# Performance work log

Measured on AMD Instinct MI355X. Metric: run time of the kernel, lower is better.

## Reference

```python
import jax, jax.numpy as jnp
import numpy as np

B, S, D, H = 2, 2048, 1024, 16
DK = D // H


def setup_inputs() -> dict:
    key = jax.random.key(0)
    ks = jax.random.split(key, 12)
    q = jax.random.normal(ks[0], (B, S, D), dtype=jnp.float32)
    k = jax.random.normal(ks[1], (B, S, D), dtype=jnp.float32)
    v = jax.random.normal(ks[2], (B, S, D), dtype=jnp.float32)
    # causal mask: 1 = attend, 0 = masked (masked_fill(mask==0, -inf))
    mask = jnp.tril(jnp.ones((S, S), dtype=jnp.int32))[None, None]
    w = 0.02
    Wq = jax.random.normal(ks[3], (D, D), dtype=jnp.float32) * w
    bq = jnp.zeros((D,), dtype=jnp.float32)
    Wk = jax.random.normal(ks[4], (D, D), dtype=jnp.float32) * w
    bk = jnp.zeros((D,), dtype=jnp.float32)
    Wv = jax.random.normal(ks[5], (D, D), dtype=jnp.float32) * w
    bv = jnp.zeros((D,), dtype=jnp.float32)
    Wo = jax.random.normal(ks[6], (D, D), dtype=jnp.float32) * w
    bo = jnp.zeros((D,), dtype=jnp.float32)
    return {"q": q, "k": k, "v": v, "mask": mask,
            "Wq": Wq, "bq": bq, "Wk": Wk, "bk": bk,
            "Wv": Wv, "bv": bv, "Wo": Wo, "bo": bo}


def _split_heads(x):
    b, s, _ = x.shape
    return x.reshape(b, s, H, DK).transpose(0, 2, 1, 3)  # [B,H,S,DK]


def reference(q, k, v, mask, Wq, bq, Wk, bk, Wv, bv, Wo, bo):
    qh = _split_heads(q @ Wq.T + bq)
    kh = _split_heads(k @ Wk.T + bk)
    vh = _split_heads(v @ Wv.T + bv)
    scale = 1.0 / jnp.sqrt(jnp.float32(DK))
    scores = jnp.einsum("bhqd,bhkd->bhqk", qh, kh) * scale  # [B,H,S,S]
    scores = jnp.where(mask == 0, -jnp.inf, scores)
    pesos = jax.nn.softmax(scores, axis=-1)
    pesos = jnp.nan_to_num(pesos, nan=0.0)  # fully-masked rows -> 0
    out = jnp.einsum("bhqk,bhkd->bhqd", pesos, vh)
    out = out.transpose(0, 2, 1, 3).reshape(q.shape[0], q.shape[1], D)
    # dropout is identity at inference
    return out @ Wo.T + bo
```

## Files before the change

kernel.cpp:

```cpp
#include <hip/hip_runtime.h>
#include <hip/hip_bf16.h>

#define B_  2
#define S_  2048
#define D_  1024
#define H_  16
#define DK_ 64

using bf16 = __hip_bfloat16;
typedef __bf16 bf16x8 __attribute__((ext_vector_type(8)));
typedef float  f32x4  __attribute__((ext_vector_type(4)));
typedef float  f32x16 __attribute__((ext_vector_type(16)));

__device__ inline void st1(float* p, float v) { *p = v; }
__device__ inline void st1(bf16*  p, float v) { *p = __float2bfloat16(v); }

__device__ inline void gll16(const bf16* g, bf16* l) {
    __builtin_amdgcn_global_load_lds(
        (const __attribute__((address_space(1))) unsigned int*)g,
        (__attribute__((address_space(3))) unsigned int*)l, 16, 0, 0);
}

__device__ inline f32x16 mfma32(bf16x8 a, bf16x8 b, f32x16 c) {
    return __builtin_amdgcn_mfma_f32_32x32x16_bf16(a, b, c, 0, 0, 0);
}

__device__ inline unsigned cvtpk(float lo, float hi) {
    unsigned r;
    asm("v_cvt_pk_bf16_f32 %0, %1, %2" : "=v"(r) : "v"(lo), "v"(hi));
    return r;
}

__device__ inline void plswap(unsigned &d, unsigned &s) {
    asm volatile("v_permlane32_swap_b32 %0, %1" : "+v"(d), "+v"(s));
}

__global__ __launch_bounds__(256) void cvt_kernel(
    const float* __restrict__ s0, const float* __restrict__ s1,
    const float* __restrict__ s2, const float* __restrict__ s3,
    const float* __restrict__ s4, const float* __restrict__ s5,
    const float* __restrict__ s6,
    bf16* __restrict__ d0, bf16* __restrict__ d1, bf16* __restrict__ d2,
    bf16* __restrict__ d3, bf16* __restrict__ d4, bf16* __restrict__ d5,
    bf16* __restrict__ d6, int nbig, int nsmall)
{
    const int z = blockIdx.y;
    const float* s; bf16* d; int n;
    switch (z) {
        case 0: s = s0; d = d0; n = nbig;   break;
        case 1: s = s1; d = d1; n = nbig;   break;
        case 2: s = s2; d = d2; n = nbig;   break;
        case 3: s = s3; d = d3; n = nsmall; break;
        case 4: s = s4; d = d4; n = nsmall; break;
        case 5: s = s5; d = d5; n = nsmall; break;
        default: s = s6; d = d6; n = nsmall; break;
    }
    const int idx = (blockIdx.x * 256 + threadIdx.x) * 4;
    if (idx < n) {
        const float4 v = *reinterpret_cast<const float4*>(s + idx);
        union { ushort4 u; __bf16 h[4]; } r;
        r.h[0] = (__bf16)v.x; r.h[1] = (__bf16)v.y;
        r.h[2] = (__bf16)v.z; r.h[3] = (__bf16)v.w;
        *reinterpret_cast<ushort4*>(d + idx) = r.u;
    }
}

template <typename TC, bool VT3, int BM>
__global__ __launch_bounds__(256, BM == 128 ? 3 : 4) void gemm_bt_kernel(
    const bf16* __restrict__ A0, const bf16* __restrict__ A1, const bf16* __restrict__ A2,
    const bf16* __restrict__ W0, const bf16* __restrict__ W1, const bf16* __restrict__ W2,
    const float* __restrict__ b0, const float* __restrict__ b1, const float* __restrict__ b2,
    TC* __restrict__ C0, TC* __restrict__ C1, TC* __restrict__ C2,
    int M, int N, int K)
{
    const int bid  = blockIdx.x;
    const int ny   = M / BM;
    const int tile = (bid & 7) * (gridDim.x >> 3) + (bid >> 3);
    const int x    = tile & 7;
    const int pair = tile >> 3;
    const int y    = pair % ny;
    const int z    = pair / ny;

    const bf16*  A    = (z == 0) ? A0 : (z == 1) ? A1 : A2;
    const bf16*  W    = (z == 0) ? W0 : (z == 1) ? W1 : W2;
    const float* bias = (z == 0) ? b0 : (z == 1) ? b1 : b2;
    TC*          C    = (z == 0) ? C0 : (z == 1) ? C1 : C2;

    __shared__ bf16 As[2][BM][32];
    __shared__ bf16 Bs[2][128][32];

    const int t    = threadIdx.x;
    const int lane = t & 63;
    const int wave = t >> 6;
    const int quad = lane >> 4;
    const int l16  = lane & 15;
    const int wm   = wave >> 1;
    const int wn   = wave & 1;

    const int m0 = y * BM;
    const int n0 = x * 128;

    constexpr int RPW = BM / 4;
    constexpr int MI  = BM / 32;
    const int ar0 = wave * RPW + (lane >> 2);
    const int br0 = wave * 32  + (lane >> 2);
    const int c0  = (lane & 3) * 8;
    const bf16* Ab = A + (size_t)(m0 + ar0) * K + c0;
    const bf16* Bb = W + (size_t)(n0 + br0) * K + c0;

    f32x4 acc[MI][4] = {};

    for (int kt = 0; kt < K; kt += 64) {
        __syncthreads();
#pragma unroll
        for (int hh = 0; hh < 2; hh++) {
            const int ko = kt + 32 * hh;
            gll16(Ab + ko, &As[hh][wave * RPW][0]);
            if constexpr (BM == 128) gll16(Ab + 16 * K + ko, &As[hh][wave * RPW + 16][0]);
            gll16(Bb + ko, &Bs[hh][wave * 32][0]);
            gll16(Bb + 16 * K + ko, &Bs[hh][wave * 32 + 16][0]);
        }
        __syncthreads();

#pragma unroll
        for (int hh = 0; hh < 2; hh++) {
            bf16x8 af[MI], bfr[4];
#pragma unroll
            for (int mi = 0; mi < MI; mi++)
                af[mi] = *reinterpret_cast<const bf16x8*>(&As[hh][wm * (BM / 2) + mi * 16 + l16][quad * 8]);
#pragma unroll
            for (int ni = 0; ni < 4; ni++)
                bfr[ni] = *reinterpret_cast<const bf16x8*>(&Bs[hh][wn * 64 + ni * 16 + l16][quad * 8]);
#pragma unroll
            for (int mi = 0; mi < MI; mi++)
#pragma unroll
                for (int ni = 0; ni < 4; ni++)
                    acc[mi][ni] = __builtin_amdgcn_mfma_f32_16x16x32_bf16(
                        af[mi], bfr[ni], acc[mi][ni], 0, 0, 0);
        }
    }

    if (VT3 && z == 2) {
#pragma unroll
        for (int ni = 0; ni < 4; ni++) {
            const int col = n0 + wn * 64 + ni * 16 + l16;
            const float bvv = bias[col];
            const int hh = col >> 6, dh = col & 63;
#pragma unroll
            for (int mi = 0; mi < MI; mi++) {
                const int rb  = m0 + wm * (BM / 2) + mi * 16 + quad * 4;
                const int bb  = rb >> 11;
                const int tok = rb & (S_ - 1);
                union { ushort4 u; __bf16 h[4]; } pk;
#pragma unroll
                for (int i = 0; i < 4; i++)
                    pk.h[i] = (__bf16)(acc[mi][ni][i] + bvv);
                bf16* vt = (bf16*)C + ((size_t)(bb * H_ + hh) * DK_ + dh) * S_ + tok;
                *reinterpret_cast<ushort4*>(vt) = pk.u;
            }
        }
    } else {
#pragma unroll
        for (int ni = 0; ni < 4; ni++) {
            const int col = n0 + wn * 64 + ni * 16 + l16;
            const float bvv = bias[col];
#pragma unroll
            for (int mi = 0; mi < MI; mi++) {
#pragma unroll
                for (int i = 0; i < 4; i++) {
                    const int row = m0 + wm * (BM / 2) + mi * 16 + quad * 4 + i;
                    st1(&C[(size_t)row * N + col], acc[mi][ni][i] + bvv);
                }
            }
        }
    }
}

__global__ __launch_bounds__(256, 2) void attn_kernel(
    const bf16* __restrict__ Qp, const bf16* __restrict__ Kp,
    const bf16* __restrict__ VT, bf16* __restrict__ AO)
{
    const int t    = threadIdx.x;
    const int lane = t & 63;
    const int wave = t >> 6;
    const int r31  = lane & 31;
    const int hl   = lane >> 5;
    const int l7   = lane & 7;

    const int bid = blockIdx.x;
    int til, hb;
    if (bid < 256) { til = 15 - (bid >> 5); hb = bid & 31; }
    else           { til = (bid - 256) >> 5; hb = (bid - 256) & 31; }
    const int h = hb & 15;
    const int b = hb >> 4;
    const size_t bh = (size_t)b * S_ * D_ + (size_t)h * DK_;
    const bf16* vtb = VT + (size_t)(b * H_ + h) * DK_ * S_;

    __shared__ bf16 Ks[2][2][64][64];
    __shared__ bf16 Vs[2][2][64][64];

    const int sR  = lane >> 3;
    const int scg = ((lane & 7) ^ sR) * 8;

    const float QSC = 0.18033688f;
    const float NEG = -1e30f;

    bf16x8 ONES;
#pragma unroll
    for (int j = 0; j < 8; j++) ONES[j] = (__bf16)1.0f;

    const int ntot = til + 1;

    bf16x8 qf[4];
    {
        const bf16* qr = Qp + bh + (size_t)(til * 128 + wave * 32 + r31) * D_ + 8 * hl;
#pragma unroll
        for (int d = 0; d < 4; d++) {
            qf[d] = *reinterpret_cast<const bf16x8*>(qr + 16 * d);
#pragma unroll
            for (int j = 0; j < 8; j++) qf[d][j] = (__bf16)((float)qf[d][j] * QSC);
        }
    }

    f32x16 oacc0 = {}, oacc1 = {}, lacc = {};

    auto stage = [&](int slot) {
        const int k0n = slot * 128;
        const int bb  = slot & 1;
#pragma unroll
        for (int half = 0; half < 2; half++) {
            const int kh = k0n + 64 * half;
#pragma unroll
            for (int j = 0; j < 2; j++) {
                const int rb = wave * 16 + j * 8;
                gll16(Kp + bh + (size_t)(kh + rb + sR) * D_ + scg, &Ks[bb][half][rb][0]);
                gll16(vtb + (size_t)(rb + sR) * S_ + kh + scg,     &Vs[bb][half][rb][0]);
            }
        }
    };

    stage(0);
    asm volatile("s_waitcnt vmcnt(0)" ::: "memory");
    __builtin_amdgcn_s_barrier();

    for (int it = 0; it < ntot; it++) {
        if (it + 1 < ntot) stage(it + 1);

        const int buf = it & 1;
        const int qw0 = til * 128 + wave * 32;

#pragma unroll
        for (int hh = 0; hh < 2; hh++) {
            const int k0 = it * 128 + 64 * hh;
            if (k0 > qw0 + 31) continue;

            f32x16 s0 = {}, s1 = {};
#pragma unroll
            for (int d = 0; d < 4; d++) {
                const int g = ((2 * d + hl) ^ l7) * 8;
                const bf16x8 kf0 = *reinterpret_cast<const bf16x8*>(&Ks[buf][hh][r31][g]);
                const bf16x8 kf1 = *reinterpret_cast<const bf16x8*>(&Ks[buf][hh][32 + r31][g]);
                s0 = mfma32(kf0, qf[d], s0);
                s1 = mfma32(kf1, qf[d], s1);
            }

            if (k0 + 63 > qw0) {
                const int qg = qw0 + r31;
                const int kb = k0 + 4 * hl;
#pragma unroll
                for (int r = 0; r < 16; r++) {
                    const int ko = (r & 3) + 8 * (r >> 2);
                    s0[r] = (kb + ko      <= qg) ? s0[r] : NEG;
                    s1[r] = (kb + 32 + ko <= qg) ? s1[r] : NEG;
                }
            }

#pragma unroll
            for (int r = 0; r < 16; r++) {
                s0[r] = __builtin_amdgcn_exp2f(s0[r]);
                s1[r] = __builtin_amdgcn_exp2f(s1[r]);
            }

            bf16x8 pa[4];
#pragma unroll
            for (int G = 0; G < 2; G++) {
#pragma unroll
                for (int tt = 0; tt < 2; tt++) {
                    unsigned a01, a23, a45, a67;
                    if (G == 0) {
                        a01 = cvtpk(s0[8*tt+0], s0[8*tt+1]);
                        a23 = cvtpk(s0[8*tt+2], s0[8*tt+3]);
                        a45 = cvtpk(s0[8*tt+4], s0[8*tt+5]);
                        a67 = cvtpk(s0[8*tt+6], s0[8*tt+7]);
                    } else {
                        a01 = cvtpk(s1[8*tt+0], s1[8*tt+1]);
                        a23 = cvtpk(s1[8*tt+2], s1[8*tt+3]);
                        a45 = cvtpk(s1[8*tt+4], s1[8*tt+5]);
                        a67 = cvtpk(s1[8*tt+6], s1[8*tt+7]);
                    }
                    plswap(a01, a45);
                    plswap(a23, a67);
                    union { unsigned u[4]; bf16x8 v; } pu;
                    pu.u[0] = a01; pu.u[1] = a23; pu.u[2] = a45; pu.u[3] = a67;
                    pa[2 * G + tt] = pu.v;
                }
            }

#pragma unroll
            for (int s = 0; s < 4; s++) {
                const int g = ((2 * s + hl) ^ l7) * 8;
                const bf16x8 vf0 = *reinterpret_cast<const bf16x8*>(&Vs[buf][hh][r31][g]);
                const bf16x8 vf1 = *reinterpret_cast<const bf16x8*>(&Vs[buf][hh][32 + r31][g]);
                oacc0 = mfma32(pa[s], vf0, oacc0);
                oacc1 = mfma32(pa[s], vf1, oacc1);
                lacc  = mfma32(pa[s], ONES, lacc);
            }
        }

        asm volatile("s_waitcnt vmcnt(0)" ::: "memory");
        __builtin_amdgcn_s_barrier();
    }

    {
        const int qb0 = til * 128 + wave * 32;
#pragma unroll
        for (int r = 0; r < 16; r++) {
            const int q = qb0 + (r & 3) + 8 * (r >> 2) + 4 * hl;
            const float inv = 1.0f / lacc[r];
            AO[bh + (size_t)q * D_ + r31]      = __float2bfloat16(oacc0[r] * inv);
            AO[bh + (size_t)q * D_ + 32 + r31] = __float2bfloat16(oacc1[r] * inv);
        }
    }
}

extern "C" void kernel_launch(void* const* d_in, const int* in_sizes, int n_in,
                              void* d_out, int out_size, void* d_ws, size_t ws_size,
                              hipStream_t stream)
{
    const float* q  = (const float*)d_in[0];
    const float* k  = (const float*)d_in[1];
    const float* v  = (const float*)d_in[2];
    const float* Wq = (const float*)d_in[4];
    const float* bq = (const float*)d_in[5];
    const float* Wk = (const float*)d_in[6];
    const float* bk = (const float*)d_in[7];
    const float* Wv = (const float*)d_in[8];
    const float* bv = (const float*)d_in[9];
    const float* Wo = (const float*)d_in[10];
    const float* bo = (const float*)d_in[11];
    float* out = (float*)d_out;

    bf16* ws = (bf16*)d_ws;
    const size_t MD = (size_t)(B_ * S_) * D_;
    const size_t WN = (size_t)D_ * D_;
    bf16* qb  = ws;
    bf16* kb  = ws + MD;
    bf16* vb  = ws + 2 * MD;
    bf16* wqb = ws + 3 * MD;
    bf16* wkb = wqb + WN;
    bf16* wvb = wkb + WN;
    bf16* wob = wvb + WN;
    bf16* Qp  = wob + WN;
    bf16* Kp  = Qp + MD;
    bf16* VT  = Kp + MD;
    bf16* AO  = Qp;

    const int M = B_ * S_;

    cvt_kernel<<<dim3((int)(MD / 4 / 256), 7), 256, 0, stream>>>(
        q, k, v, Wq, Wk, Wv, Wo, qb, kb, vb, wqb, wkb, wvb, wob,
        (int)MD, (int)WN);

    gemm_bt_kernel<bf16, true, 128><<<dim3(768), 256, 0, stream>>>(
        qb, kb, vb, wqb, wkb, wvb, bq, bk, bv, Qp, Kp, VT, M, D_, D_);

    attn_kernel<<<dim3(512), 256, 0, stream>>>(Qp, Kp, VT, AO);

    gemm_bt_kernel<float, false, 64><<<dim3(512), 256, 0, stream>>>(
        AO, AO, AO, wob, wob, wob, bo, bo, bo, out, out, out, M, D_, D_);
}
```

Measured before the change: 216.9 us.

## Fuse fp32-to-bf16 activation conversion into QKV projection GEMM loads

The QKV projection GEMM now loads the fp32 q/k/v activations straight into LDS through global_load_lds, using an XOR-swizzled column layout. It converts them to bf16 in registers with v_cvt_pk_bf16_f32 just before the MFMA. The conversion kernel now handles only the four weight matrices, which removes a full write and re-read pass over the three large activation tensors. In exchange the A tile in LDS doubles in size, which may reduce occupancy, and each fragment read adds extra LDS reads and convert instructions.

```diff
diff --git a/kernel.cpp b/kernel.cpp
--- a/kernel.cpp
+++ b/kernel.cpp
@@ -15,7 +15,7 @@
 __device__ inline void st1(float* p, float v) { *p = v; }
 __device__ inline void st1(bf16*  p, float v) { *p = __float2bfloat16(v); }
 
-__device__ inline void gll16(const bf16* g, bf16* l) {
+__device__ inline void gll16(const void* g, void* l) {
     __builtin_amdgcn_global_load_lds(
         (const __attribute__((address_space(1))) unsigned int*)g,
         (__attribute__((address_space(3))) unsigned int*)l, 16, 0, 0);
@@ -38,22 +38,16 @@
 __global__ __launch_bounds__(256) void cvt_kernel(
     const float* __restrict__ s0, const float* __restrict__ s1,
     const float* __restrict__ s2, const float* __restrict__ s3,
-    const float* __restrict__ s4, const float* __restrict__ s5,
-    const float* __restrict__ s6,
-    bf16* __restrict__ d0, bf16* __restrict__ d1, bf16* __restrict__ d2,
-    bf16* __restrict__ d3, bf16* __restrict__ d4, bf16* __restrict__ d5,
-    bf16* __restrict__ d6, int nbig, int nsmall)
+    bf16* __restrict__ d0, bf16* __restrict__ d1,
+    bf16* __restrict__ d2, bf16* __restrict__ d3, int n)
 {
     const int z = blockIdx.y;
-    const float* s; bf16* d; int n;
+    const float* s; bf16* d;
     switch (z) {
-        case 0: s = s0; d = d0; n = nbig;   break;
-        case 1: s = s1; d = d1; n = nbig;   break;
-        case 2: s = s2; d = d2; n = nbig;   break;
-        case 3: s = s3; d = d3; n = nsmall; break;
-        case 4: s = s4; d = d4; n = nsmall; break;
-        case 5: s = s5; d = d5; n = nsmall; break;
-        default: s = s6; d = d6; n = nsmall; break;
+        case 0: s = s0; d = d0; break;
+        case 1: s = s1; d = d1; break;
+        case 2: s = s2; d = d2; break;
+        default: s = s3; d = d3; break;
     }
     const int idx = (blockIdx.x * 256 + threadIdx.x) * 4;
     if (idx < n) {
@@ -65,14 +59,16 @@
     }
 }
 
-template <typename TC, bool VT3, int BM>
+template <typename TA, typename TC, bool VT3, int BM>
 __global__ __launch_bounds__(256, BM == 128 ? 3 : 4) void gemm_bt_kernel(
-    const bf16* __restrict__ A0, const bf16* __restrict__ A1, const bf16* __restrict__ A2,
+    const TA* __restrict__ A0, const TA* __restrict__ A1, const TA* __restrict__ A2,
     const bf16* __restrict__ W0, const bf16* __restrict__ W1, const bf16* __restrict__ W2,
     const float* __restrict__ b0, const float* __restrict__ b1, const float* __restrict__ b2,
     TC* __restrict__ C0, TC* __restrict__ C1, TC* __restrict__ C2,
     int M, int N, int K)
 {
+    constexpr bool AF32 = (sizeof(TA) == 4);
+
     const int bid  = blockIdx.x;
     const int ny   = M / BM;
     const int tile = (bid & 7) * (gridDim.x >> 3) + (bid >> 3);
@@ -81,12 +77,12 @@
     const int y    = pair % ny;
     const int z    = pair / ny;
 
-    const bf16*  A    = (z == 0) ? A0 : (z == 1) ? A1 : A2;
+    const TA*    A    = (z == 0) ? A0 : (z == 1) ? A1 : A2;
     const bf16*  W    = (z == 0) ? W0 : (z == 1) ? W1 : W2;
     const float* bias = (z == 0) ? b0 : (z == 1) ? b1 : b2;
     TC*          C    = (z == 0) ? C0 : (z == 1) ? C1 : C2;
 
-    __shared__ bf16 As[2][BM][32];
+    __shared__ TA   As[2][BM][32];
     __shared__ bf16 Bs[2][128][32];
 
     const int t    = threadIdx.x;
@@ -102,11 +98,13 @@
 
     constexpr int RPW = BM / 4;
     constexpr int MI  = BM / 32;
-    const int ar0 = wave * RPW + (lane >> 2);
-    const int br0 = wave * 32  + (lane >> 2);
-    const int c0  = (lane & 3) * 8;
-    const bf16* Ab = A + (size_t)(m0 + ar0) * K + c0;
-    const bf16* Bb = W + (size_t)(n0 + br0) * K + c0;
+    int ar0, ac0;
+    if constexpr (AF32) { ar0 = wave * RPW + (lane >> 3); ac0 = ((lane & 7) ^ (lane >> 3)) * 4; }
+    else                { ar0 = wave * RPW + (lane >> 2); ac0 = (lane & 3) * 8; }
+    const int br0 = wave * 32 + (lane >> 2);
+    const int bc0 = (lane & 3) * 8;
+    const TA*   Ab = A + (size_t)(m0 + ar0) * K + ac0;
+    const bf16* Bb = W + (size_t)(n0 + br0) * K + bc0;
 
     f32x4 acc[MI][4] = {};
 
@@ -115,8 +113,14 @@
 #pragma unroll
         for (int hh = 0; hh < 2; hh++) {
             const int ko = kt + 32 * hh;
-            gll16(Ab + ko, &As[hh][wave * RPW][0]);
-            if constexpr (BM == 128) gll16(Ab + 16 * K + ko, &As[hh][wave * RPW + 16][0]);
+            if constexpr (AF32) {
+#pragma unroll
+                for (int r = 0; r < RPW; r += 8)
+                    gll16(Ab + (size_t)r * K + ko, &As[hh][wave * RPW + r][0]);
+            } else {
+                gll16(Ab + ko, &As[hh][wave * RPW][0]);
+                if constexpr (BM == 128) gll16(Ab + 16 * K + ko, &As[hh][wave * RPW + 16][0]);
+            }
             gll16(Bb + ko, &Bs[hh][wave * 32][0]);
             gll16(Bb + 16 * K + ko, &Bs[hh][wave * 32 + 16][0]);
         }
@@ -126,8 +130,22 @@
         for (int hh = 0; hh < 2; hh++) {
             bf16x8 af[MI], bfr[4];
 #pragma unroll
-            for (int mi = 0; mi < MI; mi++)
-                af[mi] = *reinterpret_cast<const bf16x8*>(&As[hh][wm * (BM / 2) + mi * 16 + l16][quad * 8]);
+            for (int mi = 0; mi < MI; mi++) {
+                const int row = wm * (BM / 2) + mi * 16 + l16;
+                if constexpr (AF32) {
+                    const int sw = l16 & 7;
+                    const float4 a = *reinterpret_cast<const float4*>(
+                        &As[hh][row][((2 * quad) ^ sw) * 4]);
+                    const float4 b = *reinterpret_cast<const float4*>(
+                        &As[hh][row][((2 * quad + 1) ^ sw) * 4]);
+                    union { unsigned u[4]; bf16x8 v; } r;
+                    r.u[0] = cvtpk(a.x, a.y); r.u[1] = cvtpk(a.z, a.w);
+                    r.u[2] = cvtpk(b.x, b.y); r.u[3] = cvtpk(b.z, b.w);
+                    af[mi] = r.v;
+                } else {
+                    af[mi] = *reinterpret_cast<const bf16x8*>(&As[hh][row][quad * 8]);
+                }
+            }
 #pragma unroll
             for (int ni = 0; ni < 4; ni++)
                 bfr[ni] = *reinterpret_cast<const bf16x8*>(&Bs[hh][wn * 64 + ni * 16 + l16][quad * 8]);
@@ -353,10 +371,7 @@
     bf16* ws = (bf16*)d_ws;
     const size_t MD = (size_t)(B_ * S_) * D_;
     const size_t WN = (size_t)D_ * D_;
-    bf16* qb  = ws;
-    bf16* kb  = ws + MD;
-    bf16* vb  = ws + 2 * MD;
-    bf16* wqb = ws + 3 * MD;
+    bf16* wqb = ws;
     bf16* wkb = wqb + WN;
     bf16* wvb = wkb + WN;
     bf16* wob = wvb + WN;
@@ -367,15 +382,14 @@
 
     const int M = B_ * S_;
 
-    cvt_kernel<<<dim3((int)(MD / 4 / 256), 7), 256, 0, stream>>>(
-        q, k, v, Wq, Wk, Wv, Wo, qb, kb, vb, wqb, wkb, wvb, wob,
-        (int)MD, (int)WN);
-
-    gemm_bt_kernel<bf16, true, 128><<<dim3(768), 256, 0, stream>>>(
-        qb, kb, vb, wqb, wkb, wvb, bq, bk, bv, Qp, Kp, VT, M, D_, D_);
+    cvt_kernel<<<dim3((int)(WN / 4 / 256), 4), 256, 0, stream>>>(
+        Wq, Wk, Wv, Wo, wqb, wkb, wvb, wob, (int)WN);
+
+    gemm_bt_kernel<float, bf16, true, 128><<<dim3(768), 256, 0, stream>>>(
+        q, k, v, wqb, wkb, wvb, bq, bk, bv, Qp, Kp, VT, M, D_, D_);
 
     attn_kernel<<<dim3(512), 256, 0, stream>>>(Qp, Kp, VT, AO);
 
-    gemm_bt_kernel<float, false, 64><<<dim3(512), 256, 0, stream>>>(
+    gemm_bt_kernel<bf16, float, false, 64><<<dim3(512), 256, 0, stream>>>(
         AO, AO, AO, wob, wob, wob, bo, bo, bo, out, out, out, M, D_, D_);
 }
```

Result: slower. 233.9 us (+7.8%).
